# Optimization experiments

Measured on AMD Instinct MI355X. Metric: run time of the kernel, lower is better.

## Reference

```python
import jax, jax.numpy as jnp
import numpy as np

N = 16383        # complete binary tree, 14 levels
D_NODE = 512
D_SSM = 512
D_STATE = 16
MAX_DEPTH = 14   # number of BFS levels (depth 0..13)
LN_EPS = 1e-5


def setup_inputs() -> dict:
    key = jax.random.key(0)
    ks = jax.random.split(key, 8)
    # tree structure: parent[i] = (i-1)//2, root has parent -1; BFS order == index order
    parent = np.concatenate([np.array([-1]), (np.arange(1, N) - 1) // 2]).astype(np.int64)
    depth = np.floor(np.log2(np.arange(N) + 1)).astype(np.int32)
    s = jax.random.normal(ks[0], (N, D_NODE), jnp.float32)
    w = jax.random.uniform(ks[1], (N,), jnp.float32, minval=0.01, maxval=1.0)
    # parameters (xavier-ish scales)
    W_in = jax.random.normal(ks[2], (D_SSM, D_NODE + 1), jnp.float32) * (1.0 / np.sqrt(D_NODE + 1))
    b_in = jnp.zeros((D_SSM,), jnp.float32)
    W_delta = jax.random.normal(ks[3], (D_SSM, D_SSM), jnp.float32) * (1.0 / np.sqrt(D_SSM))
    # dt-style bias init: softplus(b) ~ dt in [1e-3, 1e-1]
    dt = jnp.exp(jax.random.uniform(ks[4], (D_SSM,), jnp.float32) * (np.log(0.1) - np.log(0.001)) + np.log(0.001))
    b_delta = dt + jnp.log(-jnp.expm1(-dt))
    W_w = jax.random.normal(ks[5], (D_SSM, 1), jnp.float32)
    b_w = jnp.zeros((D_SSM,), jnp.float32)
    A_log = jnp.log(jnp.broadcast_to(jnp.arange(1.0, D_STATE + 1.0, dtype=jnp.float32)[None, :], (D_SSM, D_STATE)))
    D = jnp.ones((D_SSM,), jnp.float32)
    W_B = jax.random.normal(ks[6], (D_STATE, D_SSM), jnp.float32) * (1.0 / np.sqrt(D_SSM))
    b_B = jnp.zeros((D_STATE,), jnp.float32)
    W_C = jax.random.normal(ks[7], (D_STATE, D_SSM), jnp.float32) * (1.0 / np.sqrt(D_SSM))
    b_C = jnp.zeros((D_STATE,), jnp.float32)
    gamma = jnp.ones((D_SSM,), jnp.float32)
    beta = jnp.zeros((D_SSM,), jnp.float32)
    return {"s": s, "w": w, "parent": jnp.asarray(parent), "depth": jnp.asarray(depth),
            "W_in": W_in, "b_in": b_in, "W_delta": W_delta, "b_delta": b_delta,
            "W_w": W_w, "b_w": b_w, "A_log": A_log, "D": D,
            "W_B": W_B, "b_B": b_B, "W_C": W_C, "b_C": b_C,
            "gamma": gamma, "beta": beta}


def reference(s, w, parent, depth, W_in, b_in, W_delta, b_delta, W_w, b_w,
              A_log, D, W_B, b_B, W_C, b_C, gamma, beta):
    n = s.shape[0]
    log_w = jnp.log(w + 1e-6)[:, None]                       # [N, 1]
    feat = jnp.concatenate([s, log_w], axis=1)               # [N, d_node+1]
    x = feat @ W_in.T + b_in                                 # [N, d_ssm]
    delta = jax.nn.softplus(x @ W_delta.T + b_delta) * jax.nn.sigmoid(log_w @ W_w.T + b_w)  # [N, d_ssm]
    A = -jnp.exp(A_log)                                      # [d_ssm, d_state]
    B = x @ W_B.T + b_B                                      # [N, d_state]
    C = x @ W_C.T + b_C                                      # [N, d_state]
    A_bar = jnp.exp(delta[:, :, None] * A[None])             # [N, d_ssm, d_state]
    Bx = (delta * x)[:, :, None] * B[:, None, :]             # [N, d_ssm, d_state]
    # level-parallel tree scan: all nodes at BFS depth l updated together
    par = jnp.maximum(parent, 0)
    has_par = (parent >= 0)[:, None, None]
    H = jnp.zeros((n, A_bar.shape[1], A_bar.shape[2]), x.dtype)
    for lvl in range(MAX_DEPTH):
        h_par = jnp.where(has_par, jnp.take(H, par, axis=0), 0.0)
        H = jnp.where((depth == lvl)[:, None, None], A_bar * h_par + Bx, H)
    Y = jnp.einsum('nds,ns->nd', H, C) + D * x               # [N, d_ssm]
    mu = jnp.mean(Y, axis=-1, keepdims=True)
    var = jnp.var(Y, axis=-1, keepdims=True)
    return (Y - mu) / jnp.sqrt(var + LN_EPS) * gamma + beta
```

## Files before the change

kernel.cpp:

```cpp
#include <hip/hip_runtime.h>
#include <hip/hip_bf16.h>
#include <math.h>

#define D_SSM 512
#define D_STATE 16
#define CKPT_BASE 511
#define CKPT_END 1023
#define N_CKPT 512
#define MPAD 16384

typedef __attribute__((ext_vector_type(8))) short short8;
typedef __attribute__((ext_vector_type(4))) float floatx4;

__device__ __forceinline__ unsigned short f2bf(float f) {
    unsigned int u = __float_as_uint(f);
    unsigned int r = (u + 0x7fffu + ((u >> 16) & 1u)) >> 16;
    return (unsigned short)r;
}
__device__ __forceinline__ float bf2f(unsigned short u) {
    return __uint_as_float(((unsigned int)u) << 16);
}
__device__ __forceinline__ void g2lds16(const void* g, void* l) {
    __builtin_amdgcn_global_load_lds(
        (const __attribute__((address_space(1))) void*)g,
        (__attribute__((address_space(3))) void*)l, 16, 0, 0);
}

__global__ __launch_bounds__(256) void prep_kernel(
    const float* __restrict__ s, const float* __restrict__ w,
    const float* __restrict__ W_in, const float* __restrict__ W_delta,
    const float* __restrict__ W_B, const float* __restrict__ W_C,
    unsigned short* __restrict__ s_bf, float* __restrict__ lw,
    unsigned short* __restrict__ Win_bf, unsigned short* __restrict__ Wd_bf,
    unsigned short* __restrict__ Wbc_bf, int Nn)
{
    const int b = blockIdx.x, t = threadIdx.x;
    if (b < MPAD) {
        unsigned int pack = 0;
        if (b < Nn) {
            float2 sv = *(const float2*)(s + (size_t)b * 512 + t * 2);
            pack = (unsigned int)f2bf(sv.x) | ((unsigned int)f2bf(sv.y) << 16);
        }
        *(unsigned int*)(s_bf + (size_t)b * 512 + t * 2) = pack;
        if (t == 0) lw[b] = (b < Nn) ? logf(w[b] + 1e-6f) : 0.f;
    } else if (b < MPAD + 512) {
        int c = b - MPAD;
        float a0 = W_in[(size_t)c * 513 + t * 2];
        float a1 = W_in[(size_t)c * 513 + t * 2 + 1];
        *(unsigned int*)(Win_bf + (size_t)c * 512 + t * 2) =
            (unsigned int)f2bf(a0) | ((unsigned int)f2bf(a1) << 16);
    } else if (b < MPAD + 1024) {
        int c = b - MPAD - 512;
        float2 wv = *(const float2*)(W_delta + (size_t)c * 512 + t * 2);
        *(unsigned int*)(Wd_bf + (size_t)c * 512 + t * 2) =
            (unsigned int)f2bf(wv.x) | ((unsigned int)f2bf(wv.y) << 16);
    } else {
        int c = b - MPAD - 1024;
        const float* src = (c < 16) ? (W_B + (size_t)c * 512) : (W_C + (size_t)(c - 16) * 512);
        float2 wv = *(const float2*)(src + t * 2);
        *(unsigned int*)(Wbc_bf + (size_t)c * 512 + t * 2) =
            (unsigned int)f2bf(wv.x) | ((unsigned int)f2bf(wv.y) << 16);
    }
}

__global__ __launch_bounds__(256) void gemm_mfma(
    const unsigned short* __restrict__ Abf,
    const unsigned short* __restrict__ Wbf,
    float* __restrict__ outf,
    unsigned short* __restrict__ outbf,
    const float* __restrict__ bias,
    const float* __restrict__ lw,
    const float* __restrict__ wcol, int wcol_stride,
    const float* __restrict__ bw,
    int mode)
{
    __shared__ __align__(16) short As[2][64 * 32];
    __shared__ __align__(16) short Bs[2][128 * 32];
    const int tid = threadIdx.x;
    const int wave = tid >> 6, lane = tid & 63;
    const int row0 = blockIdx.y * 64;
    const int col0 = blockIdx.x * 128;
    const int wr = (wave >> 1) * 32;
    const int wc = (wave & 1) * 64;

    floatx4 acc[2][4] = {};

    const int srow = lane >> 2;
    const int sg   = (lane & 3) ^ ((srow >> 1) & 3);
    const int scol = sg * 8;

    const unsigned short* Ag = Abf + (size_t)(row0 + wave * 16 + srow) * 512 + scol;
    const unsigned short* Wg0 = Wbf + (size_t)(col0 + (wave * 2 + 0) * 16 + srow) * 512 + scol;
    const unsigned short* Wg1 = Wbf + (size_t)(col0 + (wave * 2 + 1) * 16 + srow) * 512 + scol;

    {
        g2lds16(Ag, (char*)&As[0][0] + wave * 1024);
        g2lds16(Wg0, (char*)&Bs[0][0] + (wave * 2 + 0) * 1024);
        g2lds16(Wg1, (char*)&Bs[0][0] + (wave * 2 + 1) * 1024);
    }
    __syncthreads();

    for (int it = 0; it < 16; it++) {
        const int cur = it & 1;
        if (it < 15) {
            int k1 = (it + 1) * 32;
            g2lds16(Ag + k1, (char*)&As[cur ^ 1][0] + wave * 1024);
            g2lds16(Wg0 + k1, (char*)&Bs[cur ^ 1][0] + (wave * 2 + 0) * 1024);
            g2lds16(Wg1 + k1, (char*)&Bs[cur ^ 1][0] + (wave * 2 + 1) * 1024);
        }

        short8 af[2], bfr[4];
        #pragma unroll
        for (int i = 0; i < 2; i++) {
            int m = wr + i * 16 + (lane & 15);
            int gm = (lane >> 4) ^ ((m >> 1) & 3);
            af[i] = *(const short8*)&As[cur][m * 32 + gm * 8];
        }
        #pragma unroll
        for (int j = 0; j < 4; j++) {
            int n = wc + j * 16 + (lane & 15);
            int gn = (lane >> 4) ^ ((n >> 1) & 3);
            bfr[j] = *(const short8*)&Bs[cur][n * 32 + gn * 8];
        }
        #pragma unroll
        for (int i = 0; i < 2; i++)
            #pragma unroll
            for (int j = 0; j < 4; j++)
                acc[i][j] = __builtin_amdgcn_mfma_f32_16x16x32_bf16(af[i], bfr[j], acc[i][j], 0, 0, 0);
        __syncthreads();
    }

    #pragma unroll
    for (int i = 0; i < 2; i++) {
        #pragma unroll
        for (int reg = 0; reg < 4; reg++) {
            int r = row0 + wr + i * 16 + (lane >> 4) * 4 + reg;
            float lwr = lw[r];
            #pragma unroll
            for (int j = 0; j < 4; j++) {
                int c = col0 + wc + j * 16 + (lane & 15);
                float z = acc[i][j][reg] + bias[c];
                if (mode == 0) {
                    float o = z + lwr * wcol[(size_t)c * wcol_stride];
                    outbf[(size_t)r * 512 + c] = f2bf(o);
                } else {
                    float sp = (z > 15.f) ? z : log1pf(__expf(z));
                    float sg2 = 1.f / (1.f + __expf(-(lwr * wcol[c] + bw[c])));
                    outf[(size_t)r * 512 + c] = sp * sg2;
                }
            }
        }
    }
}

__global__ __launch_bounds__(256) void bc_gemm(
    const unsigned short* __restrict__ Abf,
    const unsigned short* __restrict__ Wbc,
    const float* __restrict__ b_B, const float* __restrict__ b_C,
    float* __restrict__ Bm, float* __restrict__ Cm)
{
    __shared__ __align__(16) short As[128 * 32];
    __shared__ __align__(16) short Ws[32 * 512];
    const int tid = threadIdx.x;
    const int wave = tid >> 6, lane = tid & 63;
    const int row0 = blockIdx.x * 128;
    const int wr = wave * 32;

    for (int i = 0; i < 8; i++) {
        int fg = i * 256 + tid;
        int n = fg >> 6, kgg = fg & 63;
        short8 v = *(const short8*)(Wbc + (size_t)n * 512 + kgg * 8);
        *(short8*)&Ws[n * 512 + ((kgg ^ (n & 7)) * 8)] = v;
    }

    floatx4 acc[2][2] = {};

    const int srow = lane >> 2;
    const int sgz  = (lane & 3) ^ ((srow >> 1) & 3);
    const int scol = sgz * 8;

    for (int k0 = 0; k0 < 512; k0 += 32) {
        #pragma unroll
        for (int j = 0; j < 2; j++) {
            int c = wave * 2 + j;
            int r = c * 16 + srow;
            g2lds16(Abf + (size_t)(row0 + r) * 512 + k0 + scol, (char*)As + c * 1024);
        }
        __syncthreads();

        short8 af[2], bfr[2];
        #pragma unroll
        for (int i = 0; i < 2; i++) {
            int m = wr + i * 16 + (lane & 15);
            int gm = (lane >> 4) ^ ((m >> 1) & 3);
            af[i] = *(const short8*)&As[m * 32 + gm * 8];
        }
        #pragma unroll
        for (int j = 0; j < 2; j++) {
            int n = j * 16 + (lane & 15);
            int Gg = (k0 >> 3) + (lane >> 4);
            bfr[j] = *(const short8*)&Ws[n * 512 + ((Gg ^ (n & 7)) * 8)];
        }
        #pragma unroll
        for (int i = 0; i < 2; i++)
            #pragma unroll
            for (int j = 0; j < 2; j++)
                acc[i][j] = __builtin_amdgcn_mfma_f32_16x16x32_bf16(af[i], bfr[j], acc[i][j], 0, 0, 0);
        __syncthreads();
    }

    const int s = lane & 15;
    #pragma unroll
    for (int i = 0; i < 2; i++) {
        #pragma unroll
        for (int reg = 0; reg < 4; reg++) {
            int r = row0 + wr + i * 16 + (lane >> 4) * 4 + reg;
            Bm[(size_t)r * 16 + s] = acc[i][0][reg] + b_B[s];
            Cm[(size_t)r * 16 + s] = acc[i][1][reg] + b_C[s];
        }
    }
}

__device__ __forceinline__ bool geo_check(const float* As) {
    bool ok = true;
    #pragma unroll
    for (int s = 1; s < 16; s++) {
        float want = (float)(s + 1) * As[0];
        ok = ok && (fabsf(As[s] - want) <= 1e-4f * (float)(s + 1));
    }
    return ok;
}

__global__ __launch_bounds__(256) void ckpt_kernel(
    const unsigned short* __restrict__ x_bf, const float* __restrict__ delta,
    const float* __restrict__ Bm, const float* __restrict__ A_log,
    float* __restrict__ H9)
{
    const int n9 = blockIdx.x;
    const int t = threadIdx.x;
    const int d0 = t, d1 = t + 256;

    float As0[16], As1[16], acc0[16], acc1[16];
    #pragma unroll
    for (int s = 0; s < 16; s++) {
        As0[s] = -__expf(A_log[d0 * 16 + s]);
        As1[s] = -__expf(A_log[d1 * 16 + s]);
        acc0[s] = 0.f; acc1[s] = 0.f;
    }
    const bool fast = geo_check(As0) && geo_check(As1);

    float cum0 = 0.f, cum1 = 0.f;
    int a = CKPT_BASE + n9;
    while (a >= 0) {
        float da0 = delta[(size_t)a * 512 + d0];
        float da1 = delta[(size_t)a * 512 + d1];
        float bx0 = da0 * bf2f(x_bf[(size_t)a * 512 + d0]);
        float bx1 = da1 * bf2f(x_bf[(size_t)a * 512 + d1]);
        if (fast) {
            float r0 = __expf(As0[0] * cum0);
            float r1 = __expf(As1[0] * cum1);
            float pw0 = r0, pw1 = r1;
            #pragma unroll
            for (int s = 0; s < 16; s++) {
                float Bs = Bm[a * 16 + s];
                acc0[s] = fmaf(bx0 * pw0, Bs, acc0[s]);
                acc1[s] = fmaf(bx1 * pw1, Bs, acc1[s]);
                pw0 *= r0; pw1 *= r1;
            }
        } else {
            #pragma unroll
            for (int s = 0; s < 16; s++) {
                float Bs = Bm[a * 16 + s];
                acc0[s] = fmaf(bx0 * __expf(As0[s] * cum0), Bs, acc0[s]);
                acc1[s] = fmaf(bx1 * __expf(As1[s] * cum1), Bs, acc1[s]);
            }
        }
        cum0 += da0; cum1 += da1;
        a = (a - 1) >> 1;
    }

    float* p0 = H9 + ((size_t)n9 * 512 + d0) * 16;
    float* p1 = H9 + ((size_t)n9 * 512 + d1) * 16;
    #pragma unroll
    for (int s = 0; s < 16; s++) { p0[s] = acc0[s]; p1[s] = acc1[s]; }
}

__global__ __launch_bounds__(256) void scan_shallow(
    const unsigned short* __restrict__ x_bf, const float* __restrict__ delta,
    const float* __restrict__ Bm, const float* __restrict__ Cm,
    const float* __restrict__ A_log, const float* __restrict__ Dv,
    const float* __restrict__ gamma, const float* __restrict__ beta,
    float* __restrict__ out)
{
    const int n = blockIdx.x;
    const int t = threadIdx.x;
    const int d0 = t, d1 = t + 256;

    float As0[16], As1[16], acc0[16], acc1[16];
    #pragma unroll
    for (int s = 0; s < 16; s++) {
        As0[s] = -__expf(A_log[d0 * 16 + s]);
        As1[s] = -__expf(A_log[d1 * 16 + s]);
        acc0[s] = 0.f; acc1[s] = 0.f;
    }
    const bool fast = geo_check(As0) && geo_check(As1);

    float cum0 = 0.f, cum1 = 0.f;
    int a = n;
    while (a >= 0) {
        float da0 = delta[(size_t)a * 512 + d0];
        float da1 = delta[(size_t)a * 512 + d1];
        float bx0 = da0 * bf2f(x_bf[(size_t)a * 512 + d0]);
        float bx1 = da1 * bf2f(x_bf[(size_t)a * 512 + d1]);
        if (fast) {
            float r0 = __expf(As0[0] * cum0);
            float r1 = __expf(As1[0] * cum1);
            float pw0 = r0, pw1 = r1;
            #pragma unroll
            for (int s = 0; s < 16; s++) {
                float Bs = Bm[a * 16 + s];
                acc0[s] = fmaf(bx0 * pw0, Bs, acc0[s]);
                acc1[s] = fmaf(bx1 * pw1, Bs, acc1[s]);
                pw0 *= r0; pw1 *= r1;
            }
        } else {
            #pragma unroll
            for (int s = 0; s < 16; s++) {
                float Bs = Bm[a * 16 + s];
                acc0[s] = fmaf(bx0 * __expf(As0[s] * cum0), Bs, acc0[s]);
                acc1[s] = fmaf(bx1 * __expf(As1[s] * cum1), Bs, acc1[s]);
            }
        }
        cum0 += da0; cum1 += da1;
        a = (a - 1) >> 1;
    }

    float xn0 = bf2f(x_bf[(size_t)n * 512 + d0]);
    float xn1 = bf2f(x_bf[(size_t)n * 512 + d1]);
    float y0 = Dv[d0] * xn0, y1 = Dv[d1] * xn1;
    #pragma unroll
    for (int s = 0; s < 16; s++) {
        float Cs = Cm[(size_t)n * 16 + s];
        y0 += Cs * acc0[s];
        y1 += Cs * acc1[s];
    }

    float s1 = y0 + y1;
    float s2 = y0 * y0 + y1 * y1;
    #pragma unroll
    for (int off = 32; off > 0; off >>= 1) {
        s1 += __shfl_xor(s1, off);
        s2 += __shfl_xor(s2, off);
    }
    __shared__ float red[8];
    int wid = t >> 6, lane = t & 63;
    if (lane == 0) { red[wid] = s1; red[wid + 4] = s2; }
    __syncthreads();
    float S1 = red[0] + red[1] + red[2] + red[3];
    float S2 = red[4] + red[5] + red[6] + red[7];
    float mu = S1 * (1.f / 512.f);
    float var = S2 * (1.f / 512.f) - mu * mu;
    float inv = rsqrtf(var + 1e-5f);
    out[(size_t)n * 512 + d0] = (y0 - mu) * inv * gamma[d0] + beta[d0];
    out[(size_t)n * 512 + d1] = (y1 - mu) * inv * gamma[d1] + beta[d1];
}

__global__ __launch_bounds__(512) void scan_deep(
    const unsigned short* __restrict__ x_bf, const float* __restrict__ delta,
    const float* __restrict__ Bm, const float* __restrict__ Cm,
    const float* __restrict__ H9,
    const float* __restrict__ A_log, const float* __restrict__ Dv,
    const float* __restrict__ gamma, const float* __restrict__ beta,
    float* __restrict__ out)
{
    __shared__ float Y[31][512];
    __shared__ int nid[31];
    const int p = blockIdx.x;
    const int d = threadIdx.x;
    const int a9 = CKPT_BASE + p;

    float As0 = -__expf(A_log[d * 16]);
    bool fast = true;
    #pragma unroll
    for (int s = 1; s < 16; s++) {
        float As = -__expf(A_log[d * 16 + s]);
        fast = fast && (fabsf(As - (float)(s + 1) * As0) <= 1e-4f * (float)(s + 1));
    }

    float H9v[16];
    #pragma unroll
    for (int s = 0; s < 16; s++) H9v[s] = H9[((size_t)p * 512 + d) * 16 + s];

    {
        float xv = bf2f(x_bf[(size_t)a9 * 512 + d]);
        float y = Dv[d] * xv;
        #pragma unroll
        for (int s = 0; s < 16; s++) y = fmaf(Cm[(size_t)a9 * 16 + s], H9v[s], y);
        Y[0][d] = y;
        if (d == 0) nid[0] = a9;
    }

    auto step = [&](int n, const float* Hp, float* Hc, int slot) {
        float dlt = delta[(size_t)n * 512 + d];
        float xv = bf2f(x_bf[(size_t)n * 512 + d]);
        float bx = dlt * xv;
        const float* Bn = Bm + (size_t)n * 16;
        const float* Cn = Cm + (size_t)n * 16;
        float y = Dv[d] * xv;
        if (fast) {
            float r = __expf(As0 * dlt);
            float pw = r;
            #pragma unroll
            for (int s = 0; s < 16; s++) {
                Hc[s] = fmaf(pw, Hp[s], bx * Bn[s]);
                y = fmaf(Cn[s], Hc[s], y);
                pw *= r;
            }
        } else {
            #pragma unroll
            for (int s = 0; s < 16; s++) {
                float Ab = __expf(dlt * (-__expf(A_log[d * 16 + s])));
                Hc[s] = fmaf(Ab, Hp[s], bx * Bn[s]);
                y = fmaf(Cn[s], Hc[s], y);
            }
        }
        Y[slot][d] = y;
        if (d == 0) nid[slot] = n;
    };

    float H10[16], H11[16], H12[16], H13[16];
    int slot = 1;
    #pragma unroll
    for (int c0 = 0; c0 < 2; c0++) {
        int n10 = 2 * a9 + 1 + c0;
        step(n10, H9v, H10, slot++);
        #pragma unroll
        for (int c1 = 0; c1 < 2; c1++) {
            int n11 = 2 * n10 + 1 + c1;
            step(n11, H10, H11, slot++);
            #pragma unroll
            for (int c2 = 0; c2 < 2; c2++) {
                int n12 = 2 * n11 + 1 + c2;
                step(n12, H11, H12, slot++);
                #pragma unroll
                for (int c3 = 0; c3 < 2; c3++) {
                    int n13 = 2 * n12 + 1 + c3;
                    step(n13, H12, H13, slot++);
                }
            }
        }
    }
    __syncthreads();

    const int w = d >> 6, lane = d & 63;
    for (int i = w; i < 31; i += 8) {
        int n = nid[i];
        float v[8]; float s1 = 0.f, s2 = 0.f;
        #pragma unroll
        for (int k = 0; k < 8; k++) {
            v[k] = Y[i][lane + 64 * k];
            s1 += v[k]; s2 += v[k] * v[k];
        }
        #pragma unroll
        for (int off = 32; off > 0; off >>= 1) {
            s1 += __shfl_xor(s1, off);
            s2 += __shfl_xor(s2, off);
        }
        float mu = s1 * (1.f / 512.f);
        float inv = rsqrtf(s2 * (1.f / 512.f) - mu * mu + 1e-5f);
        #pragma unroll
        for (int k = 0; k < 8; k++) {
            int ch = lane + 64 * k;
            out[(size_t)n * 512 + ch] = (v[k] - mu) * inv * gamma[ch] + beta[ch];
        }
    }
}

extern "C" void kernel_launch(void* const* d_in, const int* in_sizes, int n_in,
                              void* d_out, int out_size, void* d_ws, size_t ws_size,
                              hipStream_t stream) {
    const float* s_in   = (const float*)d_in[0];
    const float* w      = (const float*)d_in[1];
    const float* W_in    = (const float*)d_in[4];
    const float* b_in    = (const float*)d_in[5];
    const float* W_delta = (const float*)d_in[6];
    const float* b_delta = (const float*)d_in[7];
    const float* W_w     = (const float*)d_in[8];
    const float* b_w     = (const float*)d_in[9];
    const float* A_log   = (const float*)d_in[10];
    const float* Dv      = (const float*)d_in[11];
    const float* W_B     = (const float*)d_in[12];
    const float* b_B     = (const float*)d_in[13];
    const float* W_C     = (const float*)d_in[14];
    const float* b_C     = (const float*)d_in[15];
    const float* gamma   = (const float*)d_in[16];
    const float* beta    = (const float*)d_in[17];
    float* out = (float*)d_out;

    const int Nn = in_sizes[1];

    float* ws    = (float*)d_ws;
    float* lw    = ws;
    float* delta = lw + MPAD;
    float* Bm    = delta + (size_t)MPAD * 512;
    float* Cm    = Bm + (size_t)MPAD * 16;
    float* H9    = Cm + (size_t)MPAD * 16;
    unsigned short* s_bf  = (unsigned short*)(H9 + (size_t)N_CKPT * 512 * 16);
    unsigned short* x_bf  = s_bf + (size_t)MPAD * 512;
    unsigned short* Win_bf = x_bf + (size_t)MPAD * 512;
    unsigned short* Wd_bf  = Win_bf + 512 * 512;
    unsigned short* Wbc_bf = Wd_bf + 512 * 512;

    prep_kernel<<<MPAD + 1024 + 32, 256, 0, stream>>>(s_in, w, W_in, W_delta, W_B, W_C,
                                                      s_bf, lw, Win_bf, Wd_bf, Wbc_bf, Nn);

    dim3 gg(4, 256);
    gemm_mfma<<<gg, 256, 0, stream>>>(s_bf, Win_bf, nullptr, x_bf,
                                      b_in, lw, W_in + 512, 513, nullptr, 0);
    gemm_mfma<<<gg, 256, 0, stream>>>(x_bf, Wd_bf, delta, nullptr,
                                      b_delta, lw, W_w, 1, b_w, 1);

    bc_gemm<<<128, 256, 0, stream>>>(x_bf, Wbc_bf, b_B, b_C, Bm, Cm);

    ckpt_kernel<<<N_CKPT, 256, 0, stream>>>(x_bf, delta, Bm, A_log, H9);

    scan_shallow<<<CKPT_BASE, 256, 0, stream>>>(x_bf, delta, Bm, Cm, A_log, Dv,
                                                gamma, beta, out);

    scan_deep<<<N_CKPT, 512, 0, stream>>>(x_bf, delta, Bm, Cm, H9, A_log, Dv,
                                          gamma, beta, out);
}
```

Measured before the change: 263.0 us.

## Fuse checkpoint computation into deep scan, splitting at level 10

Removes the separate checkpoint kernel and its H9 workspace. Each deep-scan block now recomputes its level-10 root state directly via an ancestor walk, then scans only three more levels (15 nodes), with twice as many blocks. scan_shallow now covers levels 0-9 directly. This saves a kernel launch and the H9 global write/read, and increases block count for the deep scan. In exchange it adds redundant ancestor-walk work and more shallow nodes handled by the slower per-node path.

```diff
diff --git a/kernel.cpp b/kernel.cpp
--- a/kernel.cpp
+++ b/kernel.cpp
@@ -4,9 +4,8 @@
 
 #define D_SSM 512
 #define D_STATE 16
-#define CKPT_BASE 511
-#define CKPT_END 1023
-#define N_CKPT 512
+#define L10_BASE 1023
+#define N_L10 1024
 #define MPAD 16384
 
 typedef __attribute__((ext_vector_type(8))) short short8;
@@ -231,60 +230,6 @@
     return ok;
 }
 
-__global__ __launch_bounds__(256) void ckpt_kernel(
-    const unsigned short* __restrict__ x_bf, const float* __restrict__ delta,
-    const float* __restrict__ Bm, const float* __restrict__ A_log,
-    float* __restrict__ H9)
-{
-    const int n9 = blockIdx.x;
-    const int t = threadIdx.x;
-    const int d0 = t, d1 = t + 256;
-
-    float As0[16], As1[16], acc0[16], acc1[16];
-    #pragma unroll
-    for (int s = 0; s < 16; s++) {
-        As0[s] = -__expf(A_log[d0 * 16 + s]);
-        As1[s] = -__expf(A_log[d1 * 16 + s]);
-        acc0[s] = 0.f; acc1[s] = 0.f;
-    }
-    const bool fast = geo_check(As0) && geo_check(As1);
-
-    float cum0 = 0.f, cum1 = 0.f;
-    int a = CKPT_BASE + n9;
-    while (a >= 0) {
-        float da0 = delta[(size_t)a * 512 + d0];
-        float da1 = delta[(size_t)a * 512 + d1];
-        float bx0 = da0 * bf2f(x_bf[(size_t)a * 512 + d0]);
-        float bx1 = da1 * bf2f(x_bf[(size_t)a * 512 + d1]);
-        if (fast) {
-            float r0 = __expf(As0[0] * cum0);
-            float r1 = __expf(As1[0] * cum1);
-            float pw0 = r0, pw1 = r1;
-            #pragma unroll
-            for (int s = 0; s < 16; s++) {
-                float Bs = Bm[a * 16 + s];
-                acc0[s] = fmaf(bx0 * pw0, Bs, acc0[s]);
-                acc1[s] = fmaf(bx1 * pw1, Bs, acc1[s]);
-                pw0 *= r0; pw1 *= r1;
-            }
-        } else {
-            #pragma unroll
-            for (int s = 0; s < 16; s++) {
-                float Bs = Bm[a * 16 + s];
-                acc0[s] = fmaf(bx0 * __expf(As0[s] * cum0), Bs, acc0[s]);
-                acc1[s] = fmaf(bx1 * __expf(As1[s] * cum1), Bs, acc1[s]);
-            }
-        }
-        cum0 += da0; cum1 += da1;
-        a = (a - 1) >> 1;
-    }
-
-    float* p0 = H9 + ((size_t)n9 * 512 + d0) * 16;
-    float* p1 = H9 + ((size_t)n9 * 512 + d1) * 16;
-    #pragma unroll
-    for (int s = 0; s < 16; s++) { p0[s] = acc0[s]; p1[s] = acc1[s]; }
-}
-
 __global__ __launch_bounds__(256) void scan_shallow(
     const unsigned short* __restrict__ x_bf, const float* __restrict__ delta,
     const float* __restrict__ Bm, const float* __restrict__ Cm,
@@ -368,16 +313,15 @@
 __global__ __launch_bounds__(512) void scan_deep(
     const unsigned short* __restrict__ x_bf, const float* __restrict__ delta,
     const float* __restrict__ Bm, const float* __restrict__ Cm,
-    const float* __restrict__ H9,
     const float* __restrict__ A_log, const float* __restrict__ Dv,
     const float* __restrict__ gamma, const float* __restrict__ beta,
     float* __restrict__ out)
 {
-    __shared__ float Y[31][512];
-    __shared__ int nid[31];
+    __shared__ float Y[15][512];
+    __shared__ int nid[15];
     const int p = blockIdx.x;
     const int d = threadIdx.x;
-    const int a9 = CKPT_BASE + p;
+    const int a10 = L10_BASE + p;
 
     float As0 = -__expf(A_log[d * 16]);
     bool fast = true;
@@ -387,17 +331,42 @@
         fast = fast && (fabsf(As - (float)(s + 1) * As0) <= 1e-4f * (float)(s + 1));
     }
 
-    float H9v[16];
-    #pragma unroll
-    for (int s = 0; s < 16; s++) H9v[s] = H9[((size_t)p * 512 + d) * 16 + s];
-
+    float H10v[16];
+    #pragma unroll
+    for (int s = 0; s < 16; s++) H10v[s] = 0.f;
     {
-        float xv = bf2f(x_bf[(size_t)a9 * 512 + d]);
+        float cum = 0.f;
+        int a = a10;
+        while (a >= 0) {
+            float dlt = delta[(size_t)a * 512 + d];
+            float bx = dlt * bf2f(x_bf[(size_t)a * 512 + d]);
+            if (fast) {
+                float r = __expf(As0 * cum);
+                float pw = r;
+                #pragma unroll
+                for (int s = 0; s < 16; s++) {
+                    H10v[s] = fmaf(bx * pw, Bm[a * 16 + s], H10v[s]);
+                    pw *= r;
+                }
+            } else {
+                #pragma unroll
+                for (int s = 0; s < 16; s++) {
+                    float As = -__expf(A_log[d * 16 + s]);
+                    H10v[s] = fmaf(bx * __expf(As * cum), Bm[a * 16 + s], H10v[s]);
+                }
+            }
+            cum += dlt;
+            a = (a - 1) >> 1;
+        }
+    }
+
+    {
+        float xv = bf2f(x_bf[(size_t)a10 * 512 + d]);
         float y = Dv[d] * xv;
         #pragma unroll
-        for (int s = 0; s < 16; s++) y = fmaf(Cm[(size_t)a9 * 16 + s], H9v[s], y);
+        for (int s = 0; s < 16; s++) y = fmaf(Cm[(size_t)a10 * 16 + s], H10v[s], y);
         Y[0][d] = y;
-        if (d == 0) nid[0] = a9;
+        if (d == 0) nid[0] = a10;
     }
 
     auto step = [&](int n, const float* Hp, float* Hc, int slot) {
@@ -428,32 +397,27 @@
         if (d == 0) nid[slot] = n;
     };
 
-    float H10[16], H11[16], H12[16], H13[16];
+    float H11[16], H12[16], H13[16];
     int slot = 1;
     #pragma unroll
     for (int c0 = 0; c0 < 2; c0++) {
-        int n10 = 2 * a9 + 1 + c0;
-        step(n10, H9v, H10, slot++);
+        int n11 = 2 * a10 + 1 + c0;
+        step(n11, H10v, H11, slot++);
         #pragma unroll
         for (int c1 = 0; c1 < 2; c1++) {
-            int n11 = 2 * n10 + 1 + c1;
-            step(n11, H10, H11, slot++);
+            int n12 = 2 * n11 + 1 + c1;
+            step(n12, H11, H12, slot++);
             #pragma unroll
             for (int c2 = 0; c2 < 2; c2++) {
-                int n12 = 2 * n11 + 1 + c2;
-                step(n12, H11, H12, slot++);
-                #pragma unroll
-                for (int c3 = 0; c3 < 2; c3++) {
-                    int n13 = 2 * n12 + 1 + c3;
-                    step(n13, H12, H13, slot++);
-                }
+                int n13 = 2 * n12 + 1 + c2;
+                step(n13, H12, H13, slot++);
             }
         }
     }
     __syncthreads();
 
     const int w = d >> 6, lane = d & 63;
-    for (int i = w; i < 31; i += 8) {
+    for (int i = w; i < 15; i += 8) {
         int n = nid[i];
         float v[8]; float s1 = 0.f, s2 = 0.f;
         #pragma unroll
@@ -504,8 +468,7 @@
     float* delta = lw + MPAD;
     float* Bm    = delta + (size_t)MPAD * 512;
     float* Cm    = Bm + (size_t)MPAD * 16;
-    float* H9    = Cm + (size_t)MPAD * 16;
-    unsigned short* s_bf  = (unsigned short*)(H9 + (size_t)N_CKPT * 512 * 16);
+    unsigned short* s_bf  = (unsigned short*)(Cm + (size_t)MPAD * 16);
     unsigned short* x_bf  = s_bf + (size_t)MPAD * 512;
     unsigned short* Win_bf = x_bf + (size_t)MPAD * 512;
     unsigned short* Wd_bf  = Win_bf + 512 * 512;
@@ -522,11 +485,9 @@
 
     bc_gemm<<<128, 256, 0, stream>>>(x_bf, Wbc_bf, b_B, b_C, Bm, Cm);
 
-    ckpt_kernel<<<N_CKPT, 256, 0, stream>>>(x_bf, delta, Bm, A_log, H9);
-
-    scan_shallow<<<CKPT_BASE, 256, 0, stream>>>(x_bf, delta, Bm, Cm, A_log, Dv,
-                                                gamma, beta, out);
-
-    scan_deep<<<N_CKPT, 512, 0, stream>>>(x_bf, delta, Bm, Cm, H9, A_log, Dv,
-                                          gamma, beta, out);
-}
+    scan_shallow<<<L10_BASE, 256, 0, stream>>>(x_bf, delta, Bm, Cm, A_log, Dv,
+                                               gamma, beta, out);
+
+    scan_deep<<<N_L10, 512, 0, stream>>>(x_bf, delta, Bm, Cm, A_log, Dv,
+                                         gamma, beta, out);
+}
```

Result: no change. 263.9 us (+0.3%).
